# Performance work log

Measured on AMD Instinct MI355X. Metric: run time of the kernel, lower is better.

## Reference

```python
import jax, jax.numpy as jnp
import numpy as np

BEV_H, BEV_W, BEV_Z = 128, 128, 16
N_VOX = BEV_H * BEV_W * BEV_Z  # 262144
C = 128
N_UNMASKED = N_VOX // 4       # 65536 seed voxels (proposal > 0)
LN_EPS = 1e-5
NEG_SLOPE = 0.01


def setup_inputs() -> dict:
    key = jax.random.key(0)
    ks = jax.random.split(key, 8)
    x3d = jax.random.normal(ks[0], (1, C, N_VOX), dtype=jnp.float32)
    # disjoint unmasked/masked index sets from a permutation (proposal mask)
    perm = jax.random.permutation(ks[1], N_VOX)
    unmasked_idx = jnp.sort(perm[:N_UNMASKED]).astype(jnp.int32)
    masked_idx = jnp.sort(perm[N_UNMASKED:]).astype(jnp.int32)
    s = 0.05
    return {
        "x3d": x3d,
        "w1": jax.random.normal(ks[2], (C, C // 2), jnp.float32) * s,
        "b1": jnp.zeros((C // 2,), jnp.float32),
        "ln_g": jnp.ones((C // 2,), jnp.float32),
        "ln_b": jnp.zeros((C // 2,), jnp.float32),
        "w2": jax.random.normal(ks[3], (C // 2, C), jnp.float32) * s,
        "b2": jnp.zeros((C,), jnp.float32),
        "sdb_w": jax.random.normal(ks[4], (C, C // 2), jnp.float32) * s,
        "sdb_b": jnp.zeros((C // 2,), jnp.float32),
        "ssc_w": jax.random.normal(ks[5], (C // 2, 20), jnp.float32) * s,
        "ssc_b": jnp.zeros((20,), jnp.float32),
        "aux_w": jax.random.normal(ks[6], (C, 20), jnp.float32) * s,
        "aux_b": jnp.zeros((20,), jnp.float32),
        "unmasked_idx": unmasked_idx,
        "masked_idx": masked_idx,
    }


def _leaky(x):
    return jnp.where(x > 0, x, NEG_SLOPE * x)


def _layernorm(x, g, b):
    mu = jnp.mean(x, axis=-1, keepdims=True)
    var = jnp.mean(jnp.square(x - mu), axis=-1, keepdims=True)
    return (x - mu) * jax.lax.rsqrt(var + LN_EPS) * g + b


def reference(x3d, w1, b1, ln_g, ln_b, w2, b2, sdb_w, sdb_b, ssc_w, ssc_b,
              aux_w, aux_b, unmasked_idx, masked_idx):
    feats = x3d[0].T  # [N_vox, C]
    # gather seed (unmasked) voxel features; SGB treated as identity stand-in
    seed_feats = feats[unmasked_idx]            # [Nu, C]
    # gather masked voxel features and infill with mlp_prior:
    # Linear -> LayerNorm -> LeakyReLU -> Linear
    m = feats[masked_idx]                       # [Nm, C]
    h = _leaky(_layernorm(m @ w1 + b1, ln_g, ln_b))
    prior = h @ w2 + b2                         # [Nm, C]
    # scatter both into the dense voxel grid
    vox = jnp.zeros((N_VOX, C), x3d.dtype)
    vox = vox.at[unmasked_idx].set(seed_feats).at[masked_idx].set(prior)
    # SDB dense decode stand-in: pointwise conv C -> C/2 + LeakyReLU
    d = _leaky(vox @ sdb_w + sdb_b)             # [N_vox, C/2]
    # ssc head: per-voxel logits -> [1, 20, H, W, Z]
    ssc = d @ ssc_w + ssc_b                     # [N_vox, 20]
    ssc_logit = ssc.reshape(BEV_H, BEV_W, BEV_Z, 20).transpose(3, 0, 1, 2)[None]
    # aux sparse head on seed features
    sem_logit = seed_feats @ aux_w + aux_b      # [Nu, 20]
    return ssc_logit, sem_logit
```

## Files before the change

kernel.cpp:

```cpp
#include <hip/hip_runtime.h>
#include <hip/hip_bf16.h>


#define NVOX 262144
#define NU   65536
#define NM   196608
#define CIN  128
#define CHALF 64
#define NCLS 20
#define TR   64
#define NBLK (NVOX / TR)

#define SXS 136
#define SHS 72

#define W1F  0
#define W2F  8192
#define SDBF 16384
#define SSCF 24576
#define AUXF 26624
#define WS_WT 30720

typedef unsigned short u16;
typedef short    bf16x8 __attribute__((ext_vector_type(8)));
typedef float    f32x4  __attribute__((ext_vector_type(4)));

__device__ __forceinline__ u16 f2b(float f) {
    __hip_bfloat16 h = __float2bfloat16(f);
    return *(u16*)&h;
}

__global__ void prep_weights(const float* __restrict__ w1,  const float* __restrict__ w2,
                             const float* __restrict__ sdbw,const float* __restrict__ sscw,
                             const float* __restrict__ auxw,
                             const int* __restrict__ uidx,  const int* __restrict__ midx,
                             u16* __restrict__ ws) {
    int i = blockIdx.x * blockDim.x + threadIdx.x;
    const int stride = gridDim.x * blockDim.x;
    int* __restrict__ rank = (int*)(ws + WS_WT);
    for (int t = i; t < NU; t += stride) rank[uidx[t]] = t;
    for (int t = i; t < NM; t += stride) rank[midx[t]] = -1;
    for (; i < WS_WT; i += stride) {
        float v;
        if (i < W2F) {
            int t = i, j = t & 7, lane = (t >> 3) & 63, kc = (t >> 9) & 3, nt = t >> 11;
            int k = kc*32 + (lane >> 4)*8 + j, n = nt*16 + (lane & 15);
            v = w1[k*CHALF + n];
        } else if (i < SDBF) {
            int t = i - W2F, j = t & 7, lane = (t >> 3) & 63, kc = (t >> 9) & 1, nt = t >> 10;
            int k = kc*32 + (lane >> 4)*8 + j, n = nt*16 + (lane & 15);
            v = w2[k*CIN + n];
        } else if (i < SSCF) {
            int t = i - SDBF, j = t & 7, lane = (t >> 3) & 63, kc = (t >> 9) & 3, nt = t >> 11;
            int k = kc*32 + (lane >> 4)*8 + j, n = nt*16 + (lane & 15);
            v = sdbw[k*CHALF + n];
        } else if (i < AUXF) {
            int t = i - SSCF, j = t & 7, lane = (t >> 3) & 63, kc = (t >> 9) & 1, nt = t >> 10;
            int k = kc*32 + (lane >> 4)*8 + j, n = nt*16 + (lane & 15);
            v = (n < NCLS) ? sscw[k*NCLS + n] : 0.f;
        } else {
            int t = i - AUXF, j = t & 7, lane = (t >> 3) & 63, kc = (t >> 9) & 3, nt = t >> 11;
            int k = kc*32 + (lane >> 4)*8 + j, n = nt*16 + (lane & 15);
            v = (n < NCLS) ? auxw[k*NCLS + n] : 0.f;
        }
        ws[i] = f2b(v);
    }
}

__global__ __launch_bounds__(256, 3)
void sgn_mfma(const float* __restrict__ x3d,
              const float* __restrict__ b1,   const float* __restrict__ lng,
              const float* __restrict__ lnb,  const float* __restrict__ bb2,
              const float* __restrict__ sdbb, const float* __restrict__ sscb,
              const float* __restrict__ auxb,
              const int* __restrict__ rank,   const u16* __restrict__ wt,
              float* __restrict__ out)
{
    __shared__ __align__(16) u16 sX[TR * SXS];
    __shared__ __align__(16) u16 sH[TR * SHS];
    __shared__ __align__(16) u16 wbuf[8704];
    __shared__ int sRank[TR];

    const int tid = threadIdx.x;
    const int p0  = (int)blockIdx.x * TR;

    const int g  = tid >> 4;
    const int v0 = (tid & 15) * 4;
    f32x4 va[4], vb[4];
    #pragma unroll
    for (int i = 0; i < 4; ++i) {
        const int c0 = i*32 + g*2;
        va[i] = *(const f32x4*)&x3d[(size_t)c0      * NVOX + p0 + v0];
        vb[i] = *(const f32x4*)&x3d[(size_t)(c0+1)  * NVOX + p0 + v0];
    }

    if (tid < TR) sRank[tid] = rank[p0 + tid];

    {
        const uint4* src = (const uint4*)(wt + W1F);
        #pragma unroll
        for (int t = 0; t < 4; ++t)
            ((uint4*)wbuf)[tid + t*256] = src[tid + t*256];
    }

    #pragma unroll
    for (int i = 0; i < 4; ++i) {
        const int c0 = i*32 + g*2;
        #pragma unroll
        for (int j = 0; j < 4; ++j) {
            unsigned pk = (unsigned)f2b(va[i][j]) | ((unsigned)f2b(vb[i][j]) << 16);
            *(unsigned*)&sX[(v0 + j)*SXS + c0] = pk;
        }
    }
    __syncthreads();

    const int m0   = (tid >> 6) * 16;
    const int lane = tid & 63;
    const int q    = lane >> 4;
    const int n15  = lane & 15;
    const int kq   = q * 8;

    {
        f32x4 acc[4];
        #pragma unroll
        for (int nt = 0; nt < 4; ++nt) {
            const float b = b1[nt*16 + n15];
            acc[nt] = (f32x4){b, b, b, b};
        }
        #pragma unroll
        for (int kc = 0; kc < 4; ++kc) {
            const bf16x8 a = *(const bf16x8*)&sX[(m0 + n15) * SXS + kc*32 + kq];
            #pragma unroll
            for (int nt = 0; nt < 4; ++nt) {
                const bf16x8 b = *(const bf16x8*)&wbuf[((nt*4 + kc)*64 + lane)*8];
                acc[nt] = __builtin_amdgcn_mfma_f32_16x16x32_bf16(a, b, acc[nt], 0, 0, 0);
            }
        }
        float gv[4], ev[4];
        #pragma unroll
        for (int nt = 0; nt < 4; ++nt) { gv[nt] = lng[nt*16 + n15]; ev[nt] = lnb[nt*16 + n15]; }
        #pragma unroll
        for (int reg = 0; reg < 4; ++reg) {
            float s1 = acc[0][reg] + acc[1][reg] + acc[2][reg] + acc[3][reg];
            float s2 = acc[0][reg]*acc[0][reg] + acc[1][reg]*acc[1][reg]
                     + acc[2][reg]*acc[2][reg] + acc[3][reg]*acc[3][reg];
            #pragma unroll
            for (int m = 1; m <= 8; m <<= 1) {
                s1 += __shfl_xor(s1, m, 64);
                s2 += __shfl_xor(s2, m, 64);
            }
            const float mu  = s1 * (1.f/64.f);
            const float var = s2 * (1.f/64.f) - mu*mu;
            const float rs  = rsqrtf(var + 1e-5f);
            #pragma unroll
            for (int nt = 0; nt < 4; ++nt) {
                float h = (acc[nt][reg] - mu) * rs * gv[nt] + ev[nt];
                h = h > 0.f ? h : 0.01f*h;
                sH[(m0 + q*4 + reg) * SHS + nt*16 + n15] = f2b(h);
            }
        }
    }
    __syncthreads();

    #pragma unroll
    for (int t = 0; t < 4; ++t)
        ((uint4*)wbuf)[tid + t*256] = ((const uint4*)(wt + W2F))[tid + t*256];
    __syncthreads();

    {
        f32x4 acc2[8];
        #pragma unroll
        for (int nt = 0; nt < 8; ++nt) {
            const float b = bb2[nt*16 + n15];
            acc2[nt] = (f32x4){b, b, b, b};
        }
        #pragma unroll
        for (int kc = 0; kc < 2; ++kc) {
            const bf16x8 a = *(const bf16x8*)&sH[(m0 + n15) * SHS + kc*32 + kq];
            #pragma unroll
            for (int nt = 0; nt < 8; ++nt) {
                const bf16x8 b = *(const bf16x8*)&wbuf[((nt*2 + kc)*64 + lane)*8];
                acc2[nt] = __builtin_amdgcn_mfma_f32_16x16x32_bf16(a, b, acc2[nt], 0, 0, 0);
            }
        }
        #pragma unroll
        for (int reg = 0; reg < 4; ++reg) {
            const int row = m0 + q*4 + reg;
            if (sRank[row] < 0) {
                #pragma unroll
                for (int nt = 0; nt < 8; ++nt)
                    sX[row * SXS + nt*16 + n15] = f2b(acc2[nt][reg]);
            }
        }
    }
    __syncthreads();

    #pragma unroll
    for (int t = 0; t < 4; ++t)
        ((uint4*)wbuf)[tid + t*256] = ((const uint4*)(wt + SDBF))[tid + t*256];
    __syncthreads();

    {
        f32x4 accd[4];
        #pragma unroll
        for (int nt = 0; nt < 4; ++nt) {
            const float b = sdbb[nt*16 + n15];
            accd[nt] = (f32x4){b, b, b, b};
        }
        #pragma unroll
        for (int kc = 0; kc < 4; ++kc) {
            const bf16x8 a = *(const bf16x8*)&sX[(m0 + n15) * SXS + kc*32 + kq];
            #pragma unroll
            for (int nt = 0; nt < 4; ++nt) {
                const bf16x8 b = *(const bf16x8*)&wbuf[((nt*4 + kc)*64 + lane)*8];
                accd[nt] = __builtin_amdgcn_mfma_f32_16x16x32_bf16(a, b, accd[nt], 0, 0, 0);
            }
        }
        #pragma unroll
        for (int reg = 0; reg < 4; ++reg)
            #pragma unroll
            for (int nt = 0; nt < 4; ++nt) {
                float vv = accd[nt][reg];
                vv = vv > 0.f ? vv : 0.01f*vv;
                sH[(m0 + q*4 + reg) * SHS + nt*16 + n15] = f2b(vv);
            }
    }
    __syncthreads();

    #pragma unroll
    for (int t = 0; t < 3; ++t)
        ((uint4*)wbuf)[tid + t*256] = ((const uint4*)(wt + SSCF))[tid + t*256];
    __syncthreads();

    float* sOut = (float*)(wbuf + 6144);

    {
        f32x4 accs[2];
        #pragma unroll
        for (int nt = 0; nt < 2; ++nt) {
            const int col = nt*16 + n15;
            const float b = (col < NCLS) ? sscb[col] : 0.f;
            accs[nt] = (f32x4){b, b, b, b};
        }
        #pragma unroll
        for (int kc = 0; kc < 2; ++kc) {
            const bf16x8 a = *(const bf16x8*)&sH[(m0 + n15) * SHS + kc*32 + kq];
            #pragma unroll
            for (int nt = 0; nt < 2; ++nt) {
                const bf16x8 b = *(const bf16x8*)&wbuf[((nt*2 + kc)*64 + lane)*8];
                accs[nt] = __builtin_amdgcn_mfma_f32_16x16x32_bf16(a, b, accs[nt], 0, 0, 0);
            }
        }
        #pragma unroll
        for (int reg = 0; reg < 4; ++reg) {
            const int row = m0 + q*4 + reg;
            sOut[row*NCLS + n15] = accs[0][reg];
            if (n15 < 4) sOut[row*NCLS + 16 + n15] = accs[1][reg];
        }
    }

    f32x4 acca[2];
    {
        #pragma unroll
        for (int nt = 0; nt < 2; ++nt) {
            const int col = nt*16 + n15;
            const float b = (col < NCLS) ? auxb[col] : 0.f;
            acca[nt] = (f32x4){b, b, b, b};
        }
        #pragma unroll
        for (int kc = 0; kc < 4; ++kc) {
            const bf16x8 a = *(const bf16x8*)&sX[(m0 + n15) * SXS + kc*32 + kq];
            #pragma unroll
            for (int nt = 0; nt < 2; ++nt) {
                const bf16x8 b = *(const bf16x8*)&wbuf[2048 + ((nt*4 + kc)*64 + lane)*8];
                acca[nt] = __builtin_amdgcn_mfma_f32_16x16x32_bf16(a, b, acca[nt], 0, 0, 0);
            }
        }
    }
    __syncthreads();

    #pragma unroll
    for (int jj = 0; jj < 5; ++jj) {
        const int i = tid + jj*256;
        out[(size_t)(i >> 6) * NVOX + p0 + (i & 63)] = sOut[(i & 63) * NCLS + (i >> 6)];
    }

    {
        const size_t base = (size_t)NCLS * NVOX;
        #pragma unroll
        for (int reg = 0; reg < 4; ++reg) {
            const int row = m0 + q*4 + reg;
            const int rk  = sRank[row];
            if (rk >= 0) {
                out[base + (size_t)rk * NCLS + n15] = acca[0][reg];
                if (n15 < 4)
                    out[base + (size_t)rk * NCLS + 16 + n15] = acca[1][reg];
            }
        }
    }
}

extern "C" void kernel_launch(void* const* d_in, const int* in_sizes, int n_in,
                              void* d_out, int out_size, void* d_ws, size_t ws_size,
                              hipStream_t stream) {
    const float* x3d  = (const float*)d_in[0];
    const float* w1   = (const float*)d_in[1];
    const float* b1   = (const float*)d_in[2];
    const float* lng  = (const float*)d_in[3];
    const float* lnb  = (const float*)d_in[4];
    const float* w2   = (const float*)d_in[5];
    const float* bb2  = (const float*)d_in[6];
    const float* sdbw = (const float*)d_in[7];
    const float* sdbb = (const float*)d_in[8];
    const float* sscw = (const float*)d_in[9];
    const float* sscb = (const float*)d_in[10];
    const float* auxw = (const float*)d_in[11];
    const float* auxb = (const float*)d_in[12];
    const int*   uidx = (const int*)d_in[13];
    const int*   midx = (const int*)d_in[14];
    float* out = (float*)d_out;
    u16*   wt  = (u16*)d_ws;
    const int* rank = (const int*)((const char*)d_ws + WS_WT*2);

    hipLaunchKernelGGL(prep_weights, dim3(128), dim3(256), 0, stream,
                       w1, w2, sdbw, sscw, auxw, uidx, midx, wt);
    hipLaunchKernelGGL(sgn_mfma, dim3(NBLK), dim3(256), 0, stream,
                       x3d, b1, lng, lnb, bb2, sdbb, sscb, auxb,
                       rank, wt, out);
}
```

Measured before the change: 249.9 us.

## Read MFMA weight fragments directly from global memory and drop LDS staging barriers

Removes the shared-memory weight buffer. Each MFMA B-fragment is now loaded straight from the pre-packed global weight array, which lets the kernel drop six __syncthreads barriers between stages. Each wave only touches its own rows of sX and sH, so the barriers are not needed. With less LDS in use, launch bounds are raised to allow 4 blocks per CU, and the logits staging buffer gets a padded stride of 21 to reduce bank conflicts on the transposed store. In exchange, every wave fetches the weights through L1/L2 instead of sharing one LDS copy per block, which adds cache traffic and latency inside the MFMA loops.

```diff
diff --git a/kernel.cpp b/kernel.cpp
--- a/kernel.cpp
+++ b/kernel.cpp
@@ -13,6 +13,7 @@
 
 #define SXS 136
 #define SHS 72
+#define SOS 21
 
 #define W1F  0
 #define W2F  8192
@@ -67,7 +68,7 @@
     }
 }
 
-__global__ __launch_bounds__(256, 3)
+__global__ __launch_bounds__(256, 4)
 void sgn_mfma(const float* __restrict__ x3d,
               const float* __restrict__ b1,   const float* __restrict__ lng,
               const float* __restrict__ lnb,  const float* __restrict__ bb2,
@@ -78,7 +79,7 @@
 {
     __shared__ __align__(16) u16 sX[TR * SXS];
     __shared__ __align__(16) u16 sH[TR * SHS];
-    __shared__ __align__(16) u16 wbuf[8704];
+    __shared__ __align__(16) float sOut[TR * SOS];
     __shared__ int sRank[TR];
 
     const int tid = threadIdx.x;
@@ -96,13 +97,6 @@
 
     if (tid < TR) sRank[tid] = rank[p0 + tid];
 
-    {
-        const uint4* src = (const uint4*)(wt + W1F);
-        #pragma unroll
-        for (int t = 0; t < 4; ++t)
-            ((uint4*)wbuf)[tid + t*256] = src[tid + t*256];
-    }
-
     #pragma unroll
     for (int i = 0; i < 4; ++i) {
         const int c0 = i*32 + g*2;
@@ -120,6 +114,7 @@
     const int n15  = lane & 15;
     const int kq   = q * 8;
 
+
     {
         f32x4 acc[4];
         #pragma unroll
@@ -132,7 +127,7 @@
             const bf16x8 a = *(const bf16x8*)&sX[(m0 + n15) * SXS + kc*32 + kq];
             #pragma unroll
             for (int nt = 0; nt < 4; ++nt) {
-                const bf16x8 b = *(const bf16x8*)&wbuf[((nt*4 + kc)*64 + lane)*8];
+                const bf16x8 b = *(const bf16x8*)&wt[W1F + ((nt*4 + kc)*64 + lane)*8];
                 acc[nt] = __builtin_amdgcn_mfma_f32_16x16x32_bf16(a, b, acc[nt], 0, 0, 0);
             }
         }
@@ -160,12 +155,6 @@
             }
         }
     }
-    __syncthreads();
-
-    #pragma unroll
-    for (int t = 0; t < 4; ++t)
-        ((uint4*)wbuf)[tid + t*256] = ((const uint4*)(wt + W2F))[tid + t*256];
-    __syncthreads();
 
     {
         f32x4 acc2[8];
@@ -179,7 +168,7 @@
             const bf16x8 a = *(const bf16x8*)&sH[(m0 + n15) * SHS + kc*32 + kq];
             #pragma unroll
             for (int nt = 0; nt < 8; ++nt) {
-                const bf16x8 b = *(const bf16x8*)&wbuf[((nt*2 + kc)*64 + lane)*8];
+                const bf16x8 b = *(const bf16x8*)&wt[W2F + ((nt*2 + kc)*64 + lane)*8];
                 acc2[nt] = __builtin_amdgcn_mfma_f32_16x16x32_bf16(a, b, acc2[nt], 0, 0, 0);
             }
         }
@@ -193,12 +182,6 @@
             }
         }
     }
-    __syncthreads();
-
-    #pragma unroll
-    for (int t = 0; t < 4; ++t)
-        ((uint4*)wbuf)[tid + t*256] = ((const uint4*)(wt + SDBF))[tid + t*256];
-    __syncthreads();
 
     {
         f32x4 accd[4];
@@ -212,7 +195,7 @@
             const bf16x8 a = *(const bf16x8*)&sX[(m0 + n15) * SXS + kc*32 + kq];
             #pragma unroll
             for (int nt = 0; nt < 4; ++nt) {
-                const bf16x8 b = *(const bf16x8*)&wbuf[((nt*4 + kc)*64 + lane)*8];
+                const bf16x8 b = *(const bf16x8*)&wt[SDBF + ((nt*4 + kc)*64 + lane)*8];
                 accd[nt] = __builtin_amdgcn_mfma_f32_16x16x32_bf16(a, b, accd[nt], 0, 0, 0);
             }
         }
@@ -225,14 +208,6 @@
                 sH[(m0 + q*4 + reg) * SHS + nt*16 + n15] = f2b(vv);
             }
     }
-    __syncthreads();
-
-    #pragma unroll
-    for (int t = 0; t < 3; ++t)
-        ((uint4*)wbuf)[tid + t*256] = ((const uint4*)(wt + SSCF))[tid + t*256];
-    __syncthreads();
-
-    float* sOut = (float*)(wbuf + 6144);
 
     {
         f32x4 accs[2];
@@ -247,15 +222,15 @@
             const bf16x8 a = *(const bf16x8*)&sH[(m0 + n15) * SHS + kc*32 + kq];
             #pragma unroll
             for (int nt = 0; nt < 2; ++nt) {
-                const bf16x8 b = *(const bf16x8*)&wbuf[((nt*2 + kc)*64 + lane)*8];
+                const bf16x8 b = *(const bf16x8*)&wt[SSCF + ((nt*2 + kc)*64 + lane)*8];
                 accs[nt] = __builtin_amdgcn_mfma_f32_16x16x32_bf16(a, b, accs[nt], 0, 0, 0);
             }
         }
         #pragma unroll
         for (int reg = 0; reg < 4; ++reg) {
             const int row = m0 + q*4 + reg;
-            sOut[row*NCLS + n15] = accs[0][reg];
-            if (n15 < 4) sOut[row*NCLS + 16 + n15] = accs[1][reg];
+            sOut[row*SOS + n15] = accs[0][reg];
+            if (n15 < 4) sOut[row*SOS + 16 + n15] = accs[1][reg];
         }
     }
 
@@ -272,7 +247,7 @@
             const bf16x8 a = *(const bf16x8*)&sX[(m0 + n15) * SXS + kc*32 + kq];
             #pragma unroll
             for (int nt = 0; nt < 2; ++nt) {
-                const bf16x8 b = *(const bf16x8*)&wbuf[2048 + ((nt*4 + kc)*64 + lane)*8];
+                const bf16x8 b = *(const bf16x8*)&wt[AUXF + ((nt*4 + kc)*64 + lane)*8];
                 acca[nt] = __builtin_amdgcn_mfma_f32_16x16x32_bf16(a, b, acca[nt], 0, 0, 0);
             }
         }
@@ -282,7 +257,7 @@
     #pragma unroll
     for (int jj = 0; jj < 5; ++jj) {
         const int i = tid + jj*256;
-        out[(size_t)(i >> 6) * NVOX + p0 + (i & 63)] = sOut[(i & 63) * NCLS + (i >> 6)];
+        out[(size_t)(i >> 6) * NVOX + p0 + (i & 63)] = sOut[(i & 63) * SOS + (i >> 6)];
     }
 
     {
```

New measurement: 250.1 us. About the same (+0.1%).
